# Kernel optimization log

Measured on AMD Instinct MI355X. Metric: run time of the kernel, lower is better.

The kernel has to match this reference:

```python
import jax, jax.numpy as jnp
import numpy as np

# Config (matches init_kwargs)
V = 32000      # vocab_size
H = 1024       # hidden_size
NH = 16        # num_heads
NKV = 4        # num_kv_heads
L = 4          # num_layers
FF = 4096      # intermediate_size
MAXPOS = 2048
HD = H // NH   # head_dim = 64
KVD = H * NKV // NH  # kv projection dim = 256
EPS = 1e-5


def setup_inputs() -> dict:
    key = jax.random.key(0)
    ks = iter(jax.random.split(key, 64))
    B, T = 1, 2048
    std = 0.02

    def w(shape):
        return jax.random.normal(next(ks), shape, dtype=jnp.float32) * std

    inp = {
        "input_ids": jax.random.randint(next(ks), (B, T), 0, V),
        "attention_mask": jnp.zeros((B, T), dtype=jnp.float32),
        "tok_emb": w((V, H)),
        "pos_emb": w((MAXPOS, H)),
        # stacked per-layer params; Linear weights stored as [in, out]
        "qW": w((L, H, H)),   "qb": jnp.zeros((L, H)),
        "kW": w((L, H, KVD)), "kb": jnp.zeros((L, KVD)),
        "vW": w((L, H, KVD)), "vb": jnp.zeros((L, KVD)),
        "oW": w((L, H, H)),   "ob": jnp.zeros((L, H)),
        "m1W": w((L, H, FF)), "m1b": jnp.zeros((L, FF)),
        "m2W": w((L, FF, H)), "m2b": jnp.zeros((L, H)),
        "ln1g": jnp.ones((L, H)), "ln1b": jnp.zeros((L, H)),
        "ln2g": jnp.ones((L, H)), "ln2b": jnp.zeros((L, H)),
        "lnfg": jnp.ones((H,)),   "lnfb": jnp.zeros((H,)),
        "headW": w((H, V)),  # head: Linear(H, V, bias=False), stored [in,out]
    }
    return inp


def _layer_norm(x, g, b):
    m = jnp.mean(x, axis=-1, keepdims=True)
    v = jnp.mean(jnp.square(x - m), axis=-1, keepdims=True)
    return (x - m) * jax.lax.rsqrt(v + EPS) * g + b


def _gqa_attn(x, mask, qW, qb, kW, kb, vW, vb, oW, ob):
    B, T, _ = x.shape
    G = NH // NKV  # query groups per kv head
    q = (x @ qW + qb).reshape(B, T, NH, HD).transpose(0, 2, 1, 3)        # [B,NH,T,HD]
    q = q.reshape(B, NKV, G, T, HD)                                      # [B,NKV,G,T,HD]
    k = (x @ kW + kb).reshape(B, T, NKV, HD).transpose(0, 2, 1, 3)       # [B,NKV,T,HD]
    v = (x @ vW + vb).reshape(B, T, NKV, HD).transpose(0, 2, 1, 3)       # [B,NKV,T,HD]
    # naive full score tensor [B,NKV,G,T,T] (as in the original module)
    scores = jnp.einsum("bkgqd,bksd->bkgqs", q, k) / jnp.sqrt(jnp.float32(HD))
    scores = scores + mask[:, None, None, None, :]  # additive mask over keys
    attn = jax.nn.softmax(scores, axis=-1)
    out = jnp.einsum("bkgqs,bksd->bkgqd", attn, v)                       # [B,NKV,G,T,HD]
    out = out.reshape(B, NH, T, HD).transpose(0, 2, 1, 3).reshape(B, T, H)
    return out @ oW + ob


def reference(input_ids, attention_mask, tok_emb, pos_emb,
              qW, qb, kW, kb, vW, vb, oW, ob,
              m1W, m1b, m2W, m2b,
              ln1g, ln1b, ln2g, ln2b, lnfg, lnfb, headW):
    B, T = input_ids.shape
    x = tok_emb[input_ids] + pos_emb[jnp.arange(T)][None, :, :]  # [B,T,H]
    for i in range(L):
        h = _layer_norm(x, ln1g[i], ln1b[i])
        x = x + _gqa_attn(h, attention_mask, qW[i], qb[i], kW[i], kb[i],
                          vW[i], vb[i], oW[i], ob[i])
        h = _layer_norm(x, ln2g[i], ln2b[i])
        h = jax.nn.gelu(h @ m1W[i] + m1b[i], approximate=False) @ m2W[i] + m2b[i]
        x = x + h
    x = _layer_norm(x, lnfg, lnfb)
    logits = x @ headW  # [B,T,V]
    return logits
```

## Files before the change

kernel.cpp:

```cpp
#include <hip/hip_runtime.h>
#include <stdint.h>
#include <math.h>

typedef __attribute__((ext_vector_type(8))) short bf16x8;
typedef __attribute__((ext_vector_type(4))) short bf16x4;
typedef __attribute__((ext_vector_type(4))) float f32x4;

__device__ __forceinline__ short f2bf(float f) {
  unsigned u = __builtin_bit_cast(unsigned, f);
  unsigned r = u + 0x7fffu + ((u >> 16) & 1u);
  return (short)(r >> 16);
}

__device__ __forceinline__ f32x4 mfma16(bf16x8 a, bf16x8 b, f32x4 c) {
  return __builtin_amdgcn_mfma_f32_16x16x32_bf16(a, b, c, 0, 0, 0);
}

__device__ __forceinline__ void gload16(const void* g, void* l) {
  __builtin_amdgcn_global_load_lds((const __attribute__((address_space(1))) void*)g,
                                   (__attribute__((address_space(3))) void*)l, 16, 0, 0);
}

__device__ __forceinline__ int swz(int row, int col) {
  return row * 64 + (((col >> 3) ^ (row & 7)) << 3) + (col & 7);
}

__global__ __launch_bounds__(256) void embed_k(const int* __restrict__ ids,
                                               const float* __restrict__ tok,
                                               const float* __restrict__ pos,
                                               float* __restrict__ x) {
  const int t = threadIdx.x, w = t >> 6, lane = t & 63;
  const int row = blockIdx.x * 4 + w;
  const int id = ids[row];
#pragma unroll
  for (int i = 0; i < 4; ++i) {
    const int c = (i * 64 + lane) * 4;
    const float4 a = *reinterpret_cast<const float4*>(tok + (size_t)id * 1024 + c);
    const float4 b = *reinterpret_cast<const float4*>(pos + (size_t)row * 1024 + c);
    float4 o = make_float4(a.x + b.x, a.y + b.y, a.z + b.z, a.w + b.w);
    *reinterpret_cast<float4*>(x + (size_t)row * 1024 + c) = o;
  }
}

__global__ __launch_bounds__(256) void ln_k(const float* __restrict__ x,
                                            const float* __restrict__ gw,
                                            const float* __restrict__ bw,
                                            short* __restrict__ out) {
  const int t = threadIdx.x, w = t >> 6, lane = t & 63;
  const int row = blockIdx.x * 4 + w;
  float4 v[4];
  float s = 0.f, q = 0.f;
#pragma unroll
  for (int i = 0; i < 4; ++i) {
    v[i] = *reinterpret_cast<const float4*>(x + (size_t)row * 1024 + (i * 64 + lane) * 4);
    s += v[i].x + v[i].y + v[i].z + v[i].w;
    q += v[i].x * v[i].x + v[i].y * v[i].y + v[i].z * v[i].z + v[i].w * v[i].w;
  }
#pragma unroll
  for (int o = 32; o > 0; o >>= 1) { s += __shfl_xor(s, o); q += __shfl_xor(q, o); }
  const float mean = s * (1.f / 1024.f);
  const float var  = q * (1.f / 1024.f) - mean * mean;
  const float rstd = rsqrtf(var + 1e-5f);
#pragma unroll
  for (int i = 0; i < 4; ++i) {
    const int c = (i * 64 + lane) * 4;
    const float4 gv = *reinterpret_cast<const float4*>(gw + c);
    const float4 bv = *reinterpret_cast<const float4*>(bw + c);
    bf16x4 ov = { f2bf((v[i].x - mean) * rstd * gv.x + bv.x),
                  f2bf((v[i].y - mean) * rstd * gv.y + bv.y),
                  f2bf((v[i].z - mean) * rstd * gv.z + bv.z),
                  f2bf((v[i].w - mean) * rstd * gv.w + bv.w) };
    *reinterpret_cast<bf16x4*>(out + (size_t)row * 1024 + c) = ov;
  }
}

__global__ __launch_bounds__(256) void comb_ln(const float* __restrict__ t0,
                                               const float* __restrict__ t1,
                                               const float* __restrict__ bias,
                                               float* __restrict__ x,
                                               const float* __restrict__ gw,
                                               const float* __restrict__ bw,
                                               short* __restrict__ out) {
  const int t = threadIdx.x, w = t >> 6, lane = t & 63;
  const int row = blockIdx.x * 4 + w;
  float4 v[4];
  float s = 0.f, q = 0.f;
#pragma unroll
  for (int i = 0; i < 4; ++i) {
    const int c = (i * 64 + lane) * 4;
    const size_t o = (size_t)row * 1024 + c;
    const float4 xx = *reinterpret_cast<const float4*>(x + o);
    const float4 a  = *reinterpret_cast<const float4*>(t0 + o);
    const float4 b  = *reinterpret_cast<const float4*>(t1 + o);
    const float4 bb = *reinterpret_cast<const float4*>(bias + c);
    float4 r = make_float4(xx.x + a.x + b.x + bb.x, xx.y + a.y + b.y + bb.y,
                           xx.z + a.z + b.z + bb.z, xx.w + a.w + b.w + bb.w);
    *reinterpret_cast<float4*>(x + o) = r;
    v[i] = r;
    s += r.x + r.y + r.z + r.w;
    q += r.x * r.x + r.y * r.y + r.z * r.z + r.w * r.w;
  }
#pragma unroll
  for (int o = 32; o > 0; o >>= 1) { s += __shfl_xor(s, o); q += __shfl_xor(q, o); }
  const float mean = s * (1.f / 1024.f);
  const float var  = q * (1.f / 1024.f) - mean * mean;
  const float rstd = rsqrtf(var + 1e-5f);
#pragma unroll
  for (int i = 0; i < 4; ++i) {
    const int c = (i * 64 + lane) * 4;
    const float4 gv = *reinterpret_cast<const float4*>(gw + c);
    const float4 bv = *reinterpret_cast<const float4*>(bw + c);
    bf16x4 ov = { f2bf((v[i].x - mean) * rstd * gv.x + bv.x),
                  f2bf((v[i].y - mean) * rstd * gv.y + bv.y),
                  f2bf((v[i].z - mean) * rstd * gv.z + bv.z),
                  f2bf((v[i].w - mean) * rstd * gv.w + bv.w) };
    *reinterpret_cast<bf16x4*>(out + (size_t)row * 1024 + c) = ov;
  }
}

struct TSeg {
  const float* src; short* dst;
  unsigned long long inStride, outStride;
  int N, nbx, nbxy, rowOff, ldOut, blkEnd;
  float scale;
};
struct TTab { TSeg s[7]; };

__global__ __launch_bounds__(256) void tcvt_all(TTab tab) {
  const int b = blockIdx.x;
  int si = 0;
  while (b >= tab.s[si].blkEnd) ++si;
  const TSeg sg = tab.s[si];
  const int base = (si == 0) ? 0 : tab.s[si - 1].blkEnd;
  int lb = b - base;
  const int z = lb / sg.nbxy; lb -= z * sg.nbxy;
  const int by = lb / sg.nbx;
  const int bx = lb - by * sg.nbx;

  __shared__ float T[128][68];
  const float* Win = sg.src + (size_t)z * sg.inStride;
  short* Wout = sg.dst + (size_t)z * sg.outStride;
  const int n0 = bx * 64, k0 = by * 128;
  const int t = threadIdx.x;
  const int nc = (t & 15) * 4, kr = t >> 4;
#pragma unroll
  for (int p = 0; p < 8; ++p) {
    const float4 v = *reinterpret_cast<const float4*>(Win + (size_t)(k0 + kr + 16 * p) * sg.N + n0 + nc);
    T[kr + 16 * p][nc + 0] = v.x;
    T[kr + 16 * p][nc + 1] = v.y;
    T[kr + 16 * p][nc + 2] = v.z;
    T[kr + 16 * p][nc + 3] = v.w;
  }
  __syncthreads();
  const int n = t >> 2, ks = (t & 3) * 32;
  short tmp[32];
#pragma unroll
  for (int i = 0; i < 32; ++i) tmp[i] = f2bf(T[ks + i][n] * sg.scale);
  short* op = Wout + (size_t)(sg.rowOff + n0 + n) * sg.ldOut + k0 + ks;
#pragma unroll
  for (int c = 0; c < 4; ++c)
    *reinterpret_cast<bf16x8*>(op + c * 8) = *reinterpret_cast<bf16x8*>(tmp + c * 8);
}

__global__ __launch_bounds__(256) void bqkv_k(const float* __restrict__ qb,
                                              const float* __restrict__ kb,
                                              const float* __restrict__ vb,
                                              float* __restrict__ o) {
  int l = blockIdx.y;
  int c = blockIdx.x * 256 + threadIdx.x;
  float v;
  if (c < 1024) v = qb[l * 1024 + c] * 0.125f;
  else if (c < 1280) v = kb[l * 256 + c - 1024];
  else v = vb[l * 256 + c - 1280];
  o[l * 1536 + c] = v;
}

__global__ __launch_bounds__(256) void vtr_k(const short* __restrict__ v, int vld,
                                             short* __restrict__ vt) {
  __shared__ short T[64][80];
  const int kvh = blockIdx.y;
  const int s0 = blockIdx.x * 64;
  const int t = threadIdx.x;
  const int row = t >> 3, ch = t & 7;
#pragma unroll
  for (int p = 0; p < 2; ++p) {
    int s = row + 32 * p;
    bf16x8 vv = *reinterpret_cast<const bf16x8*>(v + (size_t)(s0 + s) * vld + kvh * 64 + ch * 8);
    *reinterpret_cast<bf16x8*>(&T[s][ch * 8]) = vv;
  }
  __syncthreads();
#pragma unroll
  for (int p = 0; p < 2; ++p) {
    int d = row + 32 * p;
    short tmp[8];
#pragma unroll
    for (int i = 0; i < 8; ++i) tmp[i] = T[ch * 8 + i][d];
    *reinterpret_cast<bf16x8*>(vt + (size_t)(kvh * 64 + d) * 2048 + s0 + ch * 8) =
        *reinterpret_cast<bf16x8*>(tmp);
  }
}

template <int EPI, int XSWZ, int TILE>
__global__ __launch_bounds__(256, 4)
void gemm_bt(const short* __restrict__ A, const short* __restrict__ Wt,
             const float* __restrict__ bias, const float* __restrict__ resid,
             void* __restrict__ out, int M, int N, int K, int kBeg, int kEnd,
             int nbOff, short* __restrict__ vt) {
  constexpr int BN   = (TILE == 0) ? 128 : 64;
  constexpr int WN   = (TILE == 0) ? 64 : 32;
  constexpr int NT   = (TILE == 0) ? 4 : 2;
  constexpr int BISS = (TILE == 0) ? 4 : 2;
  __shared__ short As[128 * 64];
  __shared__ short Bs[BN * 64];
  const int t = threadIdx.x;
  const int lane = t & 63, w = t >> 6;
  const int g = lane >> 4, r = lane & 15;
  const int wr = w >> 1, wc = w & 1;

  int bx = blockIdx.x, by = blockIdx.y;
  if (XSWZ == 1) {
    const int nbx = gridDim.x, nby = gridDim.y, nwg = nbx * nby;
    const int bid = by * nbx + bx;
    const int q = nwg >> 3, rr = nwg & 7;
    const int xcd = bid & 7, loc = bid >> 3;
    const int sw = (xcd < rr ? xcd * (q + 1) : rr * (q + 1) + (xcd - rr) * q) + loc;
    by = sw % nby; bx = sw / nby;
  }
  const int m0 = by * 128, n0 = (bx + nbOff) * BN;
  const int kShift = (int)blockIdx.z * (kEnd - kBeg);
  const size_t zOfs = (size_t)blockIdx.z * (size_t)M * (size_t)N;

  f32x4 acc[4][NT];
#pragma unroll
  for (int i = 0; i < 4; ++i)
#pragma unroll
    for (int j = 0; j < NT; ++j) { f32x4 z = {0.f, 0.f, 0.f, 0.f}; acc[i][j] = z; }

  const int srow = lane >> 3, sslot = lane & 7;

  for (int k0 = kBeg + kShift; k0 < kEnd + kShift; k0 += 64) {
#pragma unroll
    for (int i = 0; i < 4; ++i) {
      const int rowA = w * 32 + i * 8 + srow;
      const int colA = (sslot ^ (srow & 7)) << 3;
      gload16(A + (size_t)(m0 + rowA) * K + k0 + colA, &As[(w * 32 + i * 8) * 64]);
    }
#pragma unroll
    for (int i = 0; i < BISS; ++i) {
      const int rowB = w * (8 * BISS) + i * 8 + srow;
      const int colB = (sslot ^ (srow & 7)) << 3;
      gload16(Wt + (size_t)(n0 + rowB) * K + k0 + colB, &Bs[(w * (8 * BISS) + i * 8) * 64]);
    }
    __syncthreads();
#pragma unroll
    for (int kk = 0; kk < 64; kk += 32) {
      bf16x8 af[4], bfg[NT];
#pragma unroll
      for (int mt = 0; mt < 4; ++mt)
        af[mt] = *reinterpret_cast<const bf16x8*>(&As[swz(wr * 64 + mt * 16 + r, kk + g * 8)]);
#pragma unroll
      for (int nt = 0; nt < NT; ++nt)
        bfg[nt] = *reinterpret_cast<const bf16x8*>(&Bs[swz(wc * WN + nt * 16 + r, kk + g * 8)]);
#pragma unroll
      for (int mt = 0; mt < 4; ++mt)
#pragma unroll
        for (int nt = 0; nt < NT; ++nt)
          acc[mt][nt] = mfma16(af[mt], bfg[nt], acc[mt][nt]);
    }
    __syncthreads();
  }
#pragma unroll
  for (int nt = 0; nt < NT; ++nt) {
    const int col = n0 + wc * WN + nt * 16 + r;
    const float bv = (EPI == 3) ? 0.f : bias[col];
#pragma unroll
    for (int mt = 0; mt < 4; ++mt) {
      const int rowb = m0 + wr * 64 + mt * 16 + 4 * g;
      short vs[4];
#pragma unroll
      for (int j = 0; j < 4; ++j) {
        const int row = rowb + j;
        const size_t oi = (size_t)row * N + col;
        float vv = acc[mt][nt][j] + bv;
        if (EPI == 0) {
          ((short*)out)[oi] = f2bf(vv);
        } else if (EPI == 1) {
          vv = 0.5f * vv * (1.f + erff(vv * 0.70710678118654752f));
          ((short*)out)[oi] = f2bf(vv);
        } else if (EPI == 2) {
          ((float*)out)[oi] = resid[oi] + vv;
        } else if (EPI == 3) {
          ((float*)out)[oi + zOfs] = vv;
        } else {
          short bb = f2bf(vv);
          ((short*)out)[oi] = bb;
          vs[j] = bb;
        }
      }
      if (EPI == 4 && col >= 1280) {
        bf16x4 pk = { vs[0], vs[1], vs[2], vs[3] };
        *reinterpret_cast<bf16x4*>(vt + (size_t)(col - 1280) * 2048 + rowb) = pk;
      }
    }
  }
}

template <int EPI>
__global__ __launch_bounds__(256)
void gemm_k(const short* __restrict__ A, const float* __restrict__ W,
            const float* __restrict__ bias, const float* resid, void* out,
            int M, int N, int K, float scale) {
  __shared__ short As[128 * 64];
  __shared__ short Bs[128 * 64];
  const int t = threadIdx.x;
  const int lane = t & 63;
  const int g = lane >> 4, r = lane & 15;
  const int wid = t >> 6, wr = wid >> 1, wc = wid & 1;
  const int m0 = blockIdx.y * 128, n0 = blockIdx.x * 128;
  f32x4 acc[4][4];
#pragma unroll
  for (int i = 0; i < 4; ++i)
#pragma unroll
    for (int j = 0; j < 4; ++j) { f32x4 z = {0.f, 0.f, 0.f, 0.f}; acc[i][j] = z; }
  const int arow = t >> 3, ac = t & 7;
  const int bnn = t >> 1, bkh = t & 1;
  for (int k0 = 0; k0 < K; k0 += 64) {
#pragma unroll
    for (int p = 0; p < 4; ++p) {
      int row = arow + 32 * p;
      bf16x8 av = *reinterpret_cast<const bf16x8*>(A + (size_t)(m0 + row) * K + k0 + ac * 8);
      *reinterpret_cast<bf16x8*>(&As[swz(row, ac * 8)]) = av;
    }
#pragma unroll
    for (int p = 0; p < 8; ++p) {
      int kg = 4 * (bkh + 2 * p);
      const float* wp = W + (size_t)(k0 + kg) * N + n0 + bnn;
      bf16x4 wv = { f2bf(wp[0]), f2bf(wp[(size_t)N]), f2bf(wp[(size_t)2 * N]), f2bf(wp[(size_t)3 * N]) };
      *reinterpret_cast<bf16x4*>(&Bs[swz(bnn, kg)]) = wv;
    }
    __syncthreads();
#pragma unroll
    for (int kk = 0; kk < 64; kk += 32) {
      bf16x8 af[4], bfg[4];
#pragma unroll
      for (int mt = 0; mt < 4; ++mt)
        af[mt] = *reinterpret_cast<const bf16x8*>(&As[swz(wr * 64 + mt * 16 + r, kk + g * 8)]);
#pragma unroll
      for (int nt = 0; nt < 4; ++nt)
        bfg[nt] = *reinterpret_cast<const bf16x8*>(&Bs[swz(wc * 64 + nt * 16 + r, kk + g * 8)]);
#pragma unroll
      for (int mt = 0; mt < 4; ++mt)
#pragma unroll
        for (int nt = 0; nt < 4; ++nt)
          acc[mt][nt] = mfma16(af[mt], bfg[nt], acc[mt][nt]);
    }
    __syncthreads();
  }
#pragma unroll
  for (int nt = 0; nt < 4; ++nt) {
    const int col = n0 + wc * 64 + nt * 16 + r;
    const float bv = (EPI == 3) ? 0.f : bias[col];
#pragma unroll
    for (int mt = 0; mt < 4; ++mt) {
#pragma unroll
      for (int j = 0; j < 4; ++j) {
        const int row = m0 + wr * 64 + mt * 16 + 4 * g + j;
        const size_t oi = (size_t)row * N + col;
        float vv = acc[mt][nt][j] + bv;
        if (EPI == 0) {
          ((short*)out)[oi] = f2bf(vv * scale);
        } else if (EPI == 1) {
          vv = 0.5f * vv * (1.f + erff(vv * 0.70710678118654752f));
          ((short*)out)[oi] = f2bf(vv);
        } else if (EPI == 2) {
          ((float*)out)[oi] = resid[oi] + vv;
        } else {
          ((float*)out)[oi] = vv;
        }
      }
    }
  }
}

__global__ __launch_bounds__(256) void attn_k(const short* __restrict__ q, int qld,
                                              const short* __restrict__ k, int kld,
                                              const short* __restrict__ vt,
                                              const float* __restrict__ mask,
                                              short* __restrict__ o) {
  __shared__ short Ks[2][64 * 64];
  __shared__ short Vs[2][64 * 64];
  const int t = threadIdx.x, lane = t & 63, w = t >> 6;
  const int g = lane >> 4, r = lane & 15;
  const int h = blockIdx.y, qb = blockIdx.x, kvh = h >> 2;
  const int qrow = qb * 64 + w * 16 + r;

  const short* qp = q + (size_t)qrow * qld + h * 64;
  bf16x8 qf0 = *reinterpret_cast<const bf16x8*>(qp + g * 8);
  bf16x8 qf1 = *reinterpret_cast<const bf16x8*>(qp + 32 + g * 8);

  const short* kbase = k + kvh * 64;
  const short* vbase = vt + (size_t)kvh * 64 * 2048;

  f32x4 oacc[4];
#pragma unroll
  for (int i = 0; i < 4; ++i) { f32x4 z = {0.f, 0.f, 0.f, 0.f}; oacc[i] = z; }
  float m_run = -INFINITY, l_run = 0.f;

  const int srow = w * 8 + (lane >> 3), schunk = lane & 7;

#pragma unroll
  for (int p = 0; p < 2; ++p) {
    const int rr = srow + 32 * p;
    const int cc = (schunk ^ (rr & 7)) << 3;
    gload16(kbase + (size_t)rr * kld + cc, (char*)Ks + p * 4096 + w * 1024);
    gload16(vbase + (size_t)rr * 2048 + cc, (char*)Vs + p * 4096 + w * 1024);
  }
  asm volatile("s_waitcnt vmcnt(0)" ::: "memory");
  __syncthreads();

  for (int it = 0; it < 32; ++it) {
    const int cur = it & 1;
    if (it < 31) {
      const int s1 = (it + 1) * 64;
#pragma unroll
      for (int p = 0; p < 2; ++p) {
        const int rr = srow + 32 * p;
        const int cc = (schunk ^ (rr & 7)) << 3;
        gload16(kbase + (size_t)(s1 + rr) * kld + cc,
                (char*)Ks + (cur ^ 1) * 8192 + p * 4096 + w * 1024);
        gload16(vbase + (size_t)rr * 2048 + s1 + cc,
                (char*)Vs + (cur ^ 1) * 8192 + p * 4096 + w * 1024);
      }
    }
    const int s0 = it * 64;
    const short* Kc = Ks[cur];
    const short* Vc = Vs[cur];

    f32x4 sa[4];
#pragma unroll
    for (int st = 0; st < 4; ++st) {
      bf16x8 kf0 = *reinterpret_cast<const bf16x8*>(&Kc[swz(st * 16 + r, g * 8)]);
      bf16x8 kf1 = *reinterpret_cast<const bf16x8*>(&Kc[swz(st * 16 + r, 32 + g * 8)]);
      f32x4 z = {0.f, 0.f, 0.f, 0.f};
      z = mfma16(kf0, qf0, z);
      z = mfma16(kf1, qf1, z);
      sa[st] = z;
    }
    float sv[16];
    float pmax = -INFINITY;
#pragma unroll
    for (int st = 0; st < 4; ++st) {
      const float4 mv = *reinterpret_cast<const float4*>(mask + s0 + st * 16 + 4 * g);
#pragma unroll
      for (int j = 0; j < 4; ++j) {
        float xx = sa[st][j] + ((const float*)&mv)[j];
        sv[st * 4 + j] = xx;
        pmax = fmaxf(pmax, xx);
      }
    }
    pmax = fmaxf(pmax, __shfl_xor(pmax, 16));
    pmax = fmaxf(pmax, __shfl_xor(pmax, 32));
    float m_new = fmaxf(m_run, pmax);
    float corr = __expf(m_run - m_new);
    float psum = 0.f;
    short pb[16];
#pragma unroll
    for (int i = 0; i < 16; ++i) {
      float p = __expf(sv[i] - m_new);
      psum += p;
      pb[i] = f2bf(p);
    }
    psum += __shfl_xor(psum, 16);
    psum += __shfl_xor(psum, 32);
    l_run = l_run * corr + psum;
    m_run = m_new;
#pragma unroll
    for (int dt = 0; dt < 4; ++dt)
#pragma unroll
      for (int j = 0; j < 4; ++j) oacc[dt][j] *= corr;

#pragma unroll
    for (int hs = 0; hs < 2; ++hs) {
      bf16x8 pf = { pb[hs * 8 + 0], pb[hs * 8 + 1], pb[hs * 8 + 2], pb[hs * 8 + 3],
                    pb[hs * 8 + 4], pb[hs * 8 + 5], pb[hs * 8 + 6], pb[hs * 8 + 7] };
#pragma unroll
      for (int dt = 0; dt < 4; ++dt) {
        int d = dt * 16 + r;
        int c1 = 4 * g + 32 * hs;
        bf16x4 va  = *reinterpret_cast<const bf16x4*>(&Vc[swz(d, c1)]);
        bf16x4 vb2 = *reinterpret_cast<const bf16x4*>(&Vc[swz(d, c1 + 16)]);
        bf16x8 vf = { va[0], va[1], va[2], va[3], vb2[0], vb2[1], vb2[2], vb2[3] };
        oacc[dt] = mfma16(vf, pf, oacc[dt]);
      }
    }
    asm volatile("s_waitcnt vmcnt(0)" ::: "memory");
    __syncthreads();
  }
  float inv = 1.f / l_run;
#pragma unroll
  for (int dt = 0; dt < 4; ++dt) {
    bf16x4 ov = { f2bf(oacc[dt][0] * inv), f2bf(oacc[dt][1] * inv),
                  f2bf(oacc[dt][2] * inv), f2bf(oacc[dt][3] * inv) };
    *reinterpret_cast<bf16x4*>(o + (size_t)qrow * 1024 + h * 64 + dt * 16 + 4 * g) = ov;
  }
}

extern "C" void kernel_launch(void* const* d_in, const int* in_sizes, int n_in,
                              void* d_out, int out_size, void* d_ws, size_t ws_size,
                              hipStream_t stream) {
  const int*   ids   = (const int*)d_in[0];
  const float* mask  = (const float*)d_in[1];
  const float* tok   = (const float*)d_in[2];
  const float* pos   = (const float*)d_in[3];
  const float* qW    = (const float*)d_in[4];
  const float* qbias = (const float*)d_in[5];
  const float* kW    = (const float*)d_in[6];
  const float* kbias = (const float*)d_in[7];
  const float* vW    = (const float*)d_in[8];
  const float* vbias = (const float*)d_in[9];
  const float* oW    = (const float*)d_in[10];
  const float* obias = (const float*)d_in[11];
  const float* m1W   = (const float*)d_in[12];
  const float* m1b   = (const float*)d_in[13];
  const float* m2W   = (const float*)d_in[14];
  const float* m2b   = (const float*)d_in[15];
  const float* ln1g  = (const float*)d_in[16];
  const float* ln1b  = (const float*)d_in[17];
  const float* ln2g  = (const float*)d_in[18];
  const float* ln2b  = (const float*)d_in[19];
  const float* lnfg  = (const float*)d_in[20];
  const float* lnfb  = (const float*)d_in[21];
  const float* headW = (const float*)d_in[22];
  float* out = (float*)d_out;

  char* ws = (char*)d_ws;
  float* x   = (float*)ws;
  short* xb  = (short*)(ws + 8388608ull);

  const size_t OFF_QKV  = 12582912ull;
  const size_t OFF_AO   = 18874368ull;
  const size_t OFF_FF   = 23068672ull;
  const size_t OFF_BQ   = 39845888ull;
  const size_t OFF_WQKV = 39870464ull;
  const size_t OFF_WO   = 52453376ull;
  const size_t OFF_WM1  = 60841984ull;
  const size_t OFF_WM2  = 94396416ull;
  const size_t OFF_WH   = 127950848ull;
  const size_t OFF_TMP  = 193486848ull;
  const size_t NEED     = 210264064ull;

  if (ws_size >= NEED) {
    short* qkv  = (short*)(ws + OFF_QKV);
    short* ao   = (short*)(ws + OFF_AO);
    short* ff   = (short*)(ws + OFF_FF);
    short* vt   = ff;
    float* bqv  = (float*)(ws + OFF_BQ);
    short* Wqkv = (short*)(ws + OFF_WQKV);
    short* Wo   = (short*)(ws + OFF_WO);
    short* Wm1  = (short*)(ws + OFF_WM1);
    short* Wm2  = (short*)(ws + OFF_WM2);
    short* Wh   = (short*)(ws + OFF_WH);
    float* tmp0 = (float*)(ws + OFF_TMP);
    float* tmp1 = tmp0 + 2097152;

    TTab tab;
    int acc = 0;
    auto seg = [&](int i, const float* src, short* dst, size_t inS, size_t outS,
                   int N, int nbx, int nby, int nbz, int rowOff, int ldOut, float scale) {
      acc += nbx * nby * nbz;
      tab.s[i].src = src;      tab.s[i].dst = dst;
      tab.s[i].inStride = inS; tab.s[i].outStride = outS;
      tab.s[i].N = N;          tab.s[i].nbx = nbx;
      tab.s[i].nbxy = nbx * nby;
      tab.s[i].rowOff = rowOff; tab.s[i].ldOut = ldOut;
      tab.s[i].blkEnd = acc;   tab.s[i].scale = scale;
    };
    seg(0, headW, Wh,   0ull,        0ull,        32000, 500, 8, 1, 0,    1024, 1.f);
    seg(1, m1W,   Wm1,  4194304ull,  4194304ull,  4096,  64,  8, 4, 0,    1024, 1.f);
    seg(2, m2W,   Wm2,  4194304ull,  4194304ull,  1024,  16, 32, 4, 0,    4096, 1.f);
    seg(3, qW,    Wqkv, 1048576ull,  1572864ull,  1024,  16,  8, 4, 0,    1024, 0.125f);
    seg(4, oW,    Wo,   1048576ull,  1048576ull,  1024,  16,  8, 4, 0,    1024, 1.f);
    seg(5, kW,    Wqkv, 262144ull,   1572864ull,  256,   4,   8, 4, 1024, 1024, 1.f);
    seg(6, vW,    Wqkv, 262144ull,   1572864ull,  256,   4,   8, 4, 1280, 1024, 1.f);
    tcvt_all<<<acc, 256, 0, stream>>>(tab);
    bqkv_k<<<dim3(6, 4), 256, 0, stream>>>(qbias, kbias, vbias, bqv);

    embed_k<<<512, 256, 0, stream>>>(ids, tok, pos, x);

    for (int l = 0; l < 4; ++l) {
      short* Wq_l  = Wqkv + (size_t)l * 1536 * 1024;
      short* Wo_l  = Wo   + (size_t)l * 1024 * 1024;
      short* Wm1_l = Wm1  + (size_t)l * 4096 * 1024;
      short* Wm2_l = Wm2  + (size_t)l * 1024 * 4096;

      if (l == 0) {
        ln_k<<<512, 256, 0, stream>>>(x, ln1g, ln1b, xb);
      } else {
        comb_ln<<<512, 256, 0, stream>>>(tmp0, tmp1, m2b + (l - 1) * 1024, x,
                                         ln1g + l * 1024, ln1b + l * 1024, xb);
      }
      gemm_bt<4, 0, 1><<<dim3(24, 16), 256, 0, stream>>>(xb, Wq_l, bqv + l * 1536, nullptr,
                                                         qkv, 2048, 1536, 1024, 0, 1024, 0, vt);
      attn_k<<<dim3(32, 16), 256, 0, stream>>>(qkv, 1536, qkv + 1024, 1536, vt, mask, ao);
      gemm_bt<3, 1, 1><<<dim3(16, 16, 2), 256, 0, stream>>>(ao, Wo_l, nullptr, nullptr,
                                                            tmp0, 2048, 1024, 1024, 0, 512, 0, nullptr);
      comb_ln<<<512, 256, 0, stream>>>(tmp0, tmp1, obias + l * 1024, x,
                                       ln2g + l * 1024, ln2b + l * 1024, xb);
      gemm_bt<1, 1, 1><<<dim3(64, 16), 256, 0, stream>>>(xb, Wm1_l, m1b + l * 4096, nullptr,
                                                         ff, 2048, 4096, 1024, 0, 1024, 0, nullptr);
      gemm_bt<3, 1, 1><<<dim3(16, 16, 2), 256, 0, stream>>>(ff, Wm2_l, nullptr, nullptr,
                                                            tmp0, 2048, 1024, 4096, 0, 2048, 0, nullptr);
    }
    comb_ln<<<512, 256, 0, stream>>>(tmp0, tmp1, m2b + 3 * 1024, x, lnfg, lnfb, xb);
    gemm_bt<3, 1, 0><<<dim3(250, 16), 256, 0, stream>>>(xb, Wh, nullptr, nullptr,
                                                        out, 2048, 32000, 1024, 0, 1024, 0, nullptr);
  } else {
    short* qbf = (short*)(ws + (12u << 20));
    short* kbf = (short*)(ws + (16u << 20));
    short* vbf = (short*)(ws + (17u << 20));
    short* ao  = (short*)(ws + (18u << 20));
    short* ff  = (short*)(ws + (22u << 20));
    short* vtf = (short*)(ws + (38u << 20));

    embed_k<<<512, 256, 0, stream>>>(ids, tok, pos, x);
    for (int l = 0; l < 4; ++l) {
      ln_k<<<512, 256, 0, stream>>>(x, ln1g + l * 1024, ln1b + l * 1024, xb);
      gemm_k<0><<<dim3(8, 16), 256, 0, stream>>>(xb, qW + (size_t)l * 1024 * 1024,
          qbias + l * 1024, nullptr, qbf, 2048, 1024, 1024, 0.125f);
      gemm_k<0><<<dim3(2, 16), 256, 0, stream>>>(xb, kW + (size_t)l * 1024 * 256,
          kbias + l * 256, nullptr, kbf, 2048, 256, 1024, 1.f);
      gemm_k<0><<<dim3(2, 16), 256, 0, stream>>>(xb, vW + (size_t)l * 1024 * 256,
          vbias + l * 256, nullptr, vbf, 2048, 256, 1024, 1.f);
      vtr_k<<<dim3(32, 4), 256, 0, stream>>>(vbf, 256, vtf);
      attn_k<<<dim3(32, 16), 256, 0, stream>>>(qbf, 1024, kbf, 256, vtf, mask, ao);
      gemm_k<2><<<dim3(8, 16), 256, 0, stream>>>(ao, oW + (size_t)l * 1024 * 1024,
          obias + l * 1024, x, x, 2048, 1024, 1024, 1.f);
      ln_k<<<512, 256, 0, stream>>>(x, ln2g + l * 1024, ln2b + l * 1024, xb);
      gemm_k<1><<<dim3(32, 16), 256, 0, stream>>>(xb, m1W + (size_t)l * 1024 * 4096,
          m1b + l * 4096, nullptr, ff, 2048, 4096, 1024, 1.f);
      gemm_k<2><<<dim3(8, 16), 256, 0, stream>>>(ff, m2W + (size_t)l * 4096 * 1024,
          m2b + l * 1024, x, x, 2048, 1024, 4096, 1.f);
    }
    ln_k<<<512, 256, 0, stream>>>(x, lnfg, lnfb, xb);
    gemm_k<3><<<dim3(250, 16), 256, 0, stream>>>(xb, headW, nullptr, nullptr, out,
        2048, 32000, 1024, 1.f);
  }
}
```

Measured before the change: 971.9 us.

## Use 32x32x16 MFMA GEMM kernel for LM head, split into two launches

Adds a dedicated LM-head GEMM kernel built on 32x32x16 bf16 MFMA instructions with a 128x128 tile per block. It also remaps blocks across the XCDs. The head projection is split into two launches, each covering half the vocabulary columns. The aim is to raise MFMA throughput per LDS read on the largest GEMM. In exchange, the kernel has no double buffering, and its output stores stride across rows, which may be less coalesced.

```diff
diff --git a/kernel.cpp b/kernel.cpp
--- a/kernel.cpp
+++ b/kernel.cpp
@@ -5,6 +5,7 @@
 typedef __attribute__((ext_vector_type(8))) short bf16x8;
 typedef __attribute__((ext_vector_type(4))) short bf16x4;
 typedef __attribute__((ext_vector_type(4))) float f32x4;
+typedef __attribute__((ext_vector_type(16))) float f32x16;
 
 __device__ __forceinline__ short f2bf(float f) {
   unsigned u = __builtin_bit_cast(unsigned, f);
@@ -14,6 +15,9 @@
 
 __device__ __forceinline__ f32x4 mfma16(bf16x8 a, bf16x8 b, f32x4 c) {
   return __builtin_amdgcn_mfma_f32_16x16x32_bf16(a, b, c, 0, 0, 0);
+}
+__device__ __forceinline__ f32x16 mfma32(bf16x8 a, bf16x8 b, f32x16 c) {
+  return __builtin_amdgcn_mfma_f32_32x32x16_bf16(a, b, c, 0, 0, 0);
 }
 
 __device__ __forceinline__ void gload16(const void* g, void* l) {
@@ -197,6 +201,83 @@
     for (int i = 0; i < 8; ++i) tmp[i] = T[ch * 8 + i][d];
     *reinterpret_cast<bf16x8*>(vt + (size_t)(kvh * 64 + d) * 2048 + s0 + ch * 8) =
         *reinterpret_cast<bf16x8*>(tmp);
+  }
+}
+
+__global__ __launch_bounds__(256, 4)
+void gemm_h32(const short* __restrict__ A, const short* __restrict__ Wt,
+              float* __restrict__ out, int M, int N, int K, int nbOff) {
+  __shared__ short As[128 * 64];
+  __shared__ short Bs[128 * 64];
+  const int t = threadIdx.x;
+  const int lane = t & 63, w = t >> 6;
+  const int lr = lane & 31, h = lane >> 5;
+  const int wr = w >> 1, wc = w & 1;
+
+  int bx = blockIdx.x, by = blockIdx.y;
+  {
+    const int nbx = gridDim.x, nby = gridDim.y, nwg = nbx * nby;
+    const int bid = by * nbx + bx;
+    const int q = nwg >> 3, rr = nwg & 7;
+    const int xcd = bid & 7, loc = bid >> 3;
+    const int sw = (xcd < rr ? xcd * (q + 1) : rr * (q + 1) + (xcd - rr) * q) + loc;
+    by = sw % nby; bx = sw / nby;
+  }
+  const int m0 = by * 128, n0 = (bx + nbOff) * 128;
+
+  f32x16 acc[2][2];
+#pragma unroll
+  for (int i = 0; i < 2; ++i)
+#pragma unroll
+    for (int j = 0; j < 2; ++j)
+#pragma unroll
+      for (int e = 0; e < 16; ++e) acc[i][j][e] = 0.f;
+
+  const int srow = lane >> 3, sslot = lane & 7;
+
+  for (int k0 = 0; k0 < K; k0 += 64) {
+#pragma unroll
+    for (int i = 0; i < 4; ++i) {
+      const int rowA = w * 32 + i * 8 + srow;
+      const int colA = (sslot ^ (srow & 7)) << 3;
+      gload16(A + (size_t)(m0 + rowA) * K + k0 + colA, &As[(w * 32 + i * 8) * 64]);
+    }
+#pragma unroll
+    for (int i = 0; i < 4; ++i) {
+      const int rowB = w * 32 + i * 8 + srow;
+      const int colB = (sslot ^ (srow & 7)) << 3;
+      gload16(Wt + (size_t)(n0 + rowB) * K + k0 + colB, &Bs[(w * 32 + i * 8) * 64]);
+    }
+    __syncthreads();
+#pragma unroll
+    for (int ks = 0; ks < 4; ++ks) {
+      bf16x8 af[2], bfr[2];
+#pragma unroll
+      for (int mt = 0; mt < 2; ++mt)
+        af[mt] = *reinterpret_cast<const bf16x8*>(&As[swz(wr * 64 + mt * 32 + lr, ks * 16 + 8 * h)]);
+#pragma unroll
+      for (int nt = 0; nt < 2; ++nt)
+        bfr[nt] = *reinterpret_cast<const bf16x8*>(&Bs[swz(wc * 64 + nt * 32 + lr, ks * 16 + 8 * h)]);
+#pragma unroll
+      for (int mt = 0; mt < 2; ++mt)
+#pragma unroll
+        for (int nt = 0; nt < 2; ++nt)
+          acc[mt][nt] = mfma32(af[mt], bfr[nt], acc[mt][nt]);
+    }
+    __syncthreads();
+  }
+#pragma unroll
+  for (int nt = 0; nt < 2; ++nt) {
+    const int col = n0 + wc * 64 + nt * 32 + lr;
+#pragma unroll
+    for (int mt = 0; mt < 2; ++mt) {
+      const int rb = m0 + wr * 64 + mt * 32 + 4 * h;
+#pragma unroll
+      for (int reg = 0; reg < 16; ++reg) {
+        const int row = rb + (reg & 3) + 8 * (reg >> 2);
+        out[(size_t)row * N + col] = acc[mt][nt][reg];
+      }
+    }
   }
 }
 
@@ -612,8 +693,8 @@
                                                             tmp0, 2048, 1024, 4096, 0, 2048, 0, nullptr);
     }
     comb_ln<<<512, 256, 0, stream>>>(tmp0, tmp1, m2b + 3 * 1024, x, lnfg, lnfb, xb);
-    gemm_bt<3, 1, 0><<<dim3(250, 16), 256, 0, stream>>>(xb, Wh, nullptr, nullptr,
-                                                        out, 2048, 32000, 1024, 0, 1024, 0, nullptr);
+    gemm_h32<<<dim3(125, 16), 256, 0, stream>>>(xb, Wh, out, 2048, 32000, 1024, 0);
+    gemm_h32<<<dim3(125, 16), 256, 0, stream>>>(xb, Wh, out, 2048, 32000, 1024, 125);
   } else {
     short* qbf = (short*)(ws + (12u << 20));
     short* kbf = (short*)(ws + (16u << 20));
```

Result: no change. 988.3 us (+1.7%).
